# Performance work log

Hardware: AMD Instinct MI355X
Metric: run time of the kernel (lower is better)

The kernel has to match this reference:

```python
import jax, jax.numpy as jnp
import numpy as np

N_HEADS = 8

def setup_inputs() -> dict:
    key = jax.random.key(0)
    qkv = jax.random.normal(key, (4, 1536, 2048), dtype=jnp.float32)
    return {"qkv": qkv}

def reference(qkv):
    bs, width, length = qkv.shape
    ch = width // (3 * N_HEADS)
    q, k, v = jnp.split(qkv, 3, axis=1)  # each [bs, H*C, T]
    scale = 1.0 / np.sqrt(ch).astype(np.float32)
    q = (q * scale).reshape(bs * N_HEADS, ch, length)
    k = k.reshape(bs * N_HEADS, ch, length)
    v = v.reshape(bs * N_HEADS, ch, length)
    weight = jnp.einsum('bct,bcs->bts', q, k)  # [bs*H, T, T]
    weight = jax.nn.softmax(weight.astype(jnp.float32), axis=-1).astype(weight.dtype)
    a = jnp.einsum('bts,bcs->bct', weight, v)  # [bs*H, C, T]
    return a.reshape(bs, -1, length)
```

## Files before the change

kernel.cpp:

```cpp
#include <hip/hip_runtime.h>
#include <hip/hip_bf16.h>

typedef unsigned short u16;
typedef unsigned int uint;
typedef __bf16 bf16x8 __attribute__((ext_vector_type(8)));
typedef float f32x16 __attribute__((ext_vector_type(16)));

#define SEQ 2048
#define DH  64

__device__ __forceinline__ u16 f2bf(float x) {
  __bf16 h = (__bf16)x;
  return __builtin_bit_cast(u16, h);
}

__global__ __launch_bounds__(256) void transpose_qk(const float* __restrict__ qkv,
                                                    u16* __restrict__ qT,
                                                    u16* __restrict__ kT) {
  int idx = blockIdx.x;
  int which = idx >> 10;
  int bh = (idx >> 5) & 31;
  int t0 = (idx & 31) * 64;
  int b = bh >> 3, h = bh & 7;
  const float* src = qkv + ((size_t)(b*1536 + which*512 + h*64)) * SEQ;
  u16* dst = (which ? kT : qT) + (size_t)bh * SEQ * DH;
  float scale = which ? 1.0f : 0.1803368801111244f;

  __shared__ float tile[64][65];
  int tl = threadIdx.x & 63;
  int cw = threadIdx.x >> 6;
#pragma unroll
  for (int i = 0; i < 16; ++i) {
    int c = cw + 4*i;
    tile[c][tl] = src[(size_t)c*SEQ + t0 + tl] * scale;
  }
  __syncthreads();
  int cl2 = (threadIdx.x & 31) * 2;
  int tw  = threadIdx.x >> 5;
#pragma unroll
  for (int i = 0; i < 8; ++i) {
    int t = tw + 8*i;
    unsigned int lo = f2bf(tile[cl2][t]);
    unsigned int hi = f2bf(tile[cl2+1][t]);
    *(unsigned int*)(dst + (size_t)(t0 + t)*DH + cl2) = lo | (hi << 16);
  }
}

__global__ __launch_bounds__(256) void convert_v(const float* __restrict__ qkv,
                                                 u16* __restrict__ v) {
  int row = blockIdx.x;
  int bh = row >> 6, c = row & 63;
  int b = bh >> 3, h = bh & 7;
  const float4* src = (const float4*)(qkv + ((size_t)(b*1536 + 1024 + h*64 + c)) * SEQ);
  u16* dst = v + (size_t)row * SEQ;
  int tid = threadIdx.x;
  float4 a = src[tid*2];
  float4 bq = src[tid*2+1];
  union { u16 u[8]; int4 v4; } pk;
  pk.u[0]=f2bf(a.x); pk.u[1]=f2bf(a.y); pk.u[2]=f2bf(a.z); pk.u[3]=f2bf(a.w);
  pk.u[4]=f2bf(bq.x); pk.u[5]=f2bf(bq.y); pk.u[6]=f2bf(bq.z); pk.u[7]=f2bf(bq.w);
  *(int4*)(dst + tid*8) = pk.v4;
}

__global__ __launch_bounds__(256) void attn(const u16* __restrict__ qT,
                                            const u16* __restrict__ kT,
                                            const u16* __restrict__ vB,
                                            float* __restrict__ out) {
  const int lb = (blockIdx.x & 7) * 64 + (blockIdx.x >> 3);
  const int bh = lb >> 4;
  const int t0 = (lb & 15) * 128;
  const int tid  = threadIdx.x;
  const int wave = tid >> 6;
  const int lane = tid & 63;
  const int l31  = lane & 31;
  const int hi   = lane >> 5;

  __shared__ __align__(16) u16 kbuf[2][64*64];
  __shared__ __align__(16) u16 vbuf[2][64*64];

  const u16* qrow = qT + ((size_t)bh*SEQ + (t0 + wave*32 + l31)) * DH;
  bf16x8 bq[4];
#pragma unroll
  for (int kb = 0; kb < 4; ++kb) bq[kb] = *(const bf16x8*)(qrow + kb*16 + hi*8);

  const u16* ksrc0 = kT + (size_t)bh*SEQ*DH;
  const u16* vsrc0 = vB + (size_t)bh*DH*SEQ;
  const int ci0 = (wave*2+0)*64 + lane;
  const int ci1 = (wave*2+1)*64 + lane;
  const int kr0 = ci0 >> 3, kc0 = ci0 & 7;
  const int kr1 = ci1 >> 3, kc1 = ci1 & 7;
  const u16* kg0 = ksrc0 + (size_t)kr0*DH + ((kc0 ^ (kr0 & 7)) * 8);
  const u16* kg1 = ksrc0 + (size_t)kr1*DH + ((kc1 ^ (kr1 & 7)) * 8);
  const u16* vg0 = vsrc0 + (size_t)kr0*SEQ + ((kc0 ^ (kr0 & 7)) * 8);
  const u16* vg1 = vsrc0 + (size_t)kr1*SEQ + ((kc1 ^ (kr1 & 7)) * 8);

#define STAGE(b, s0) do {                                                         \
    __builtin_amdgcn_global_load_lds(                                             \
      (const __attribute__((address_space(1))) unsigned int*)(kg0 + (size_t)(s0)*DH), \
      (__attribute__((address_space(3))) unsigned int*)(&kbuf[b][(wave*2+0)*512]), 16, 0, 0); \
    __builtin_amdgcn_global_load_lds(                                             \
      (const __attribute__((address_space(1))) unsigned int*)(kg1 + (size_t)(s0)*DH), \
      (__attribute__((address_space(3))) unsigned int*)(&kbuf[b][(wave*2+1)*512]), 16, 0, 0); \
    __builtin_amdgcn_global_load_lds(                                             \
      (const __attribute__((address_space(1))) unsigned int*)(vg0 + (s0)),        \
      (__attribute__((address_space(3))) unsigned int*)(&vbuf[b][(wave*2+0)*512]), 16, 0, 0); \
    __builtin_amdgcn_global_load_lds(                                             \
      (const __attribute__((address_space(1))) unsigned int*)(vg1 + (s0)),        \
      (__attribute__((address_space(3))) unsigned int*)(&vbuf[b][(wave*2+1)*512]), 16, 0, 0); \
  } while (0)

  f32x16 acc0 = {}, acc1 = {};
  float m_run = -3.0e38f, l_run = 0.f;

  STAGE(0, 0);
  __syncthreads();

  int buf = 0;
  for (int s0 = 0; s0 < SEQ; s0 += 64) {
    if (s0 + 64 < SEQ) STAGE(buf ^ 1, s0 + 64);

    const u16* kb_ = kbuf[buf];
    f32x16 S0 = {}, S1 = {};
    __builtin_amdgcn_s_setprio(1);
#pragma unroll
    for (int kb = 0; kb < 4; ++kb) {
      bf16x8 a0 = *(const bf16x8*)(kb_ + l31*64      + (((2*kb+hi) ^ (l31 & 7)) * 8));
      bf16x8 a1 = *(const bf16x8*)(kb_ + (32+l31)*64 + (((2*kb+hi) ^ (l31 & 7)) * 8));
      S0 = __builtin_amdgcn_mfma_f32_32x32x16_bf16(a0, bq[kb], S0, 0, 0, 0);
      S1 = __builtin_amdgcn_mfma_f32_32x32x16_bf16(a1, bq[kb], S1, 0, 0, 0);
    }
    __builtin_amdgcn_s_setprio(0);

    float vmax = S0[0];
#pragma unroll
    for (int i = 1; i < 16; ++i) vmax = fmaxf(vmax, S0[i]);
#pragma unroll
    for (int i = 0; i < 16; ++i) vmax = fmaxf(vmax, S1[i]);
    vmax = fmaxf(vmax, __shfl_xor(vmax, 32));

    if (!__all(vmax - m_run <= 8.0f)) {
      float m_new = fmaxf(m_run, vmax);
      float alpha = __builtin_amdgcn_exp2f(m_run - m_new);
      l_run *= alpha;
#pragma unroll
      for (int i = 0; i < 16; ++i) { acc0[i] *= alpha; acc1[i] *= alpha; }
      m_run = m_new;
    }

    float p0[16], p1[16];
    float ls = 0.f;
#pragma unroll
    for (int i = 0; i < 16; ++i) { p0[i] = __builtin_amdgcn_exp2f(S0[i] - m_run); ls += p0[i]; }
#pragma unroll
    for (int i = 0; i < 16; ++i) { p1[i] = __builtin_amdgcn_exp2f(S1[i] - m_run); ls += p1[i]; }
    ls += __shfl_xor(ls, 32);
    l_run += ls;

    uint d0[8], d1[8];
#pragma unroll
    for (int q = 0; q < 4; ++q)
#pragma unroll
      for (int e = 0; e < 2; ++e) {
        asm("v_cvt_pk_bf16_f32 %0, %1, %2" : "=v"(d0[2*q+e]) : "v"(p0[4*q+2*e]), "v"(p0[4*q+2*e+1]));
        asm("v_cvt_pk_bf16_f32 %0, %1, %2" : "=v"(d1[2*q+e]) : "v"(p1[4*q+2*e]), "v"(p1[4*q+2*e+1]));
      }
    bf16x8 pf[4];
#pragma unroll
    for (int st2 = 0; st2 < 2; ++st2)
#pragma unroll
      for (int kb2 = 0; kb2 < 2; ++kb2) {
        uint X0 = (st2 ? d1 : d0)[4*kb2+0], X1 = (st2 ? d1 : d0)[4*kb2+1];
        uint Y0 = (st2 ? d1 : d0)[4*kb2+2], Y1 = (st2 ? d1 : d0)[4*kb2+3];
        asm("v_permlane32_swap_b32 %0, %1" : "+v"(X0), "+v"(Y0));
        asm("v_permlane32_swap_b32 %0, %1" : "+v"(X1), "+v"(Y1));
        uint4 u = {X0, X1, Y0, Y1};
        pf[st2*2+kb2] = __builtin_bit_cast(bf16x8, u);
      }

    const u16* vb_ = vbuf[buf];
    __builtin_amdgcn_s_setprio(1);
#pragma unroll
    for (int ks = 0; ks < 4; ++ks) {
      bf16x8 a0 = *(const bf16x8*)(vb_ + l31*64      + (((2*ks+hi) ^ (l31 & 7)) * 8));
      bf16x8 a1 = *(const bf16x8*)(vb_ + (32+l31)*64 + (((2*ks+hi) ^ (l31 & 7)) * 8));
      acc0 = __builtin_amdgcn_mfma_f32_32x32x16_bf16(a0, pf[ks], acc0, 0, 0, 0);
      acc1 = __builtin_amdgcn_mfma_f32_32x32x16_bf16(a1, pf[ks], acc1, 0, 0, 0);
    }
    __builtin_amdgcn_s_setprio(0);

    __syncthreads();
    buf ^= 1;
  }
#undef STAGE

  float linv = 1.0f / l_run;
  float* ob = out + (size_t)(bh*64) * SEQ + t0 + wave*32 + l31;
#pragma unroll
  for (int r = 0; r < 16; ++r) {
    int c0 = (r & 3) + 8*(r >> 2) + 4*hi;
    ob[(size_t)c0 * SEQ]        = acc0[r] * linv;
    ob[(size_t)(32 + c0) * SEQ] = acc1[r] * linv;
  }
}

extern "C" void kernel_launch(void* const* d_in, const int* in_sizes, int n_in,
                              void* d_out, int out_size, void* d_ws, size_t ws_size,
                              hipStream_t stream) {
  const float* qkv = (const float*)d_in[0];
  float* out = (float*)d_out;
  u16* qT = (u16*)d_ws;
  u16* kT = qT + (size_t)32*SEQ*DH;
  u16* vB = kT + (size_t)32*SEQ*DH;
  transpose_qk<<<2048, 256, 0, stream>>>(qkv, qT, kT);
  convert_v<<<2048, 256, 0, stream>>>(qkv, vB);
  attn<<<512, 256, 0, stream>>>(qT, kT, vB, out);
}
```

Measured before the change: 74.47 us.

## Halve attention block to two waves, double grid, change LDS swizzle, tree reductions

The attention kernel now runs 128-thread blocks covering 64 query rows each, with twice as many blocks. This is meant to spread work over more CUs and improve occupancy, at the cost of each block loading the K/V tiles for fewer queries and so doing more redundant global traffic. The K/V staging is rewritten so each wave issues four loads per tile, and the LDS XOR swizzle now uses a different function of the row index. The max and sum reductions become tree reductions to shorten their dependency chains.

```diff
diff --git a/kernel.cpp b/kernel.cpp
--- a/kernel.cpp
+++ b/kernel.cpp
@@ -13,6 +13,8 @@
   __bf16 h = (__bf16)x;
   return __builtin_bit_cast(u16, h);
 }
+
+#define FSW(r) ((((r) & 3) << 1) | (((r) >> 2) & 1))
 
 __global__ __launch_bounds__(256) void transpose_qk(const float* __restrict__ qkv,
                                                     u16* __restrict__ qT,
@@ -62,15 +64,15 @@
   *(int4*)(dst + tid*8) = pk.v4;
 }
 
-__global__ __launch_bounds__(256) void attn(const u16* __restrict__ qT,
+__global__ __launch_bounds__(128) void attn(const u16* __restrict__ qT,
                                             const u16* __restrict__ kT,
                                             const u16* __restrict__ vB,
                                             float* __restrict__ out) {
-  const int lb = (blockIdx.x & 7) * 64 + (blockIdx.x >> 3);
-  const int bh = lb >> 4;
-  const int t0 = (lb & 15) * 128;
+  const int lb = (blockIdx.x & 7) * 128 + (blockIdx.x >> 3);
+  const int bh = lb >> 5;
+  const int t0 = (lb & 31) * 64;
   const int tid  = threadIdx.x;
-  const int wave = tid >> 6;
+  const int wv   = tid >> 6;
   const int lane = tid & 63;
   const int l31  = lane & 31;
   const int hi   = lane >> 5;
@@ -78,39 +80,41 @@
   __shared__ __align__(16) u16 kbuf[2][64*64];
   __shared__ __align__(16) u16 vbuf[2][64*64];
 
-  const u16* qrow = qT + ((size_t)bh*SEQ + (t0 + wave*32 + l31)) * DH;
+  const u16* qrow = qT + ((size_t)bh*SEQ + (t0 + wv*32 + l31)) * DH;
   bf16x8 bq[4];
 #pragma unroll
   for (int kb = 0; kb < 4; ++kb) bq[kb] = *(const bf16x8*)(qrow + kb*16 + hi*8);
 
   const u16* ksrc0 = kT + (size_t)bh*SEQ*DH;
   const u16* vsrc0 = vB + (size_t)bh*DH*SEQ;
-  const int ci0 = (wave*2+0)*64 + lane;
-  const int ci1 = (wave*2+1)*64 + lane;
-  const int kr0 = ci0 >> 3, kc0 = ci0 & 7;
-  const int kr1 = ci1 >> 3, kc1 = ci1 & 7;
-  const u16* kg0 = ksrc0 + (size_t)kr0*DH + ((kc0 ^ (kr0 & 7)) * 8);
-  const u16* kg1 = ksrc0 + (size_t)kr1*DH + ((kc1 ^ (kr1 & 7)) * 8);
-  const u16* vg0 = vsrc0 + (size_t)kr0*SEQ + ((kc0 ^ (kr0 & 7)) * 8);
-  const u16* vg1 = vsrc0 + (size_t)kr1*SEQ + ((kc1 ^ (kr1 & 7)) * 8);
-
-#define STAGE(b, s0) do {                                                         \
-    __builtin_amdgcn_global_load_lds(                                             \
-      (const __attribute__((address_space(1))) unsigned int*)(kg0 + (size_t)(s0)*DH), \
-      (__attribute__((address_space(3))) unsigned int*)(&kbuf[b][(wave*2+0)*512]), 16, 0, 0); \
-    __builtin_amdgcn_global_load_lds(                                             \
-      (const __attribute__((address_space(1))) unsigned int*)(kg1 + (size_t)(s0)*DH), \
-      (__attribute__((address_space(3))) unsigned int*)(&kbuf[b][(wave*2+1)*512]), 16, 0, 0); \
-    __builtin_amdgcn_global_load_lds(                                             \
-      (const __attribute__((address_space(1))) unsigned int*)(vg0 + (s0)),        \
-      (__attribute__((address_space(3))) unsigned int*)(&vbuf[b][(wave*2+0)*512]), 16, 0, 0); \
-    __builtin_amdgcn_global_load_lds(                                             \
-      (const __attribute__((address_space(1))) unsigned int*)(vg1 + (s0)),        \
-      (__attribute__((address_space(3))) unsigned int*)(&vbuf[b][(wave*2+1)*512]), 16, 0, 0); \
+  const int r3  = lane >> 3;
+  const int kcc = lane & 7;
+  const int krb = wv*32 + r3;
+  const int fsw = FSW(r3);
+  const u16* kg  = ksrc0 + (size_t)krb*DH + ((kcc ^ fsw) * 8);
+  const u16* vg0 = vsrc0 + (size_t)(krb     )*SEQ + ((kcc ^ fsw) * 8);
+  const u16* vg1 = vsrc0 + (size_t)(krb +  8)*SEQ + ((kcc ^ fsw) * 8);
+  const u16* vg2 = vsrc0 + (size_t)(krb + 16)*SEQ + ((kcc ^ fsw) * 8);
+  const u16* vg3 = vsrc0 + (size_t)(krb + 24)*SEQ + ((kcc ^ fsw) * 8);
+
+#define GLDS(src, dst) __builtin_amdgcn_global_load_lds(                        \
+    (const __attribute__((address_space(1))) unsigned int*)(src),               \
+    (__attribute__((address_space(3))) unsigned int*)(dst), 16, 0, 0)
+#define STAGE(b, s0) do {                                                       \
+    GLDS(kg + (size_t)(s0)*DH,           &kbuf[b][(wv*4+0)*512]);               \
+    GLDS(kg + (size_t)(s0)*DH +  8*DH,   &kbuf[b][(wv*4+1)*512]);               \
+    GLDS(kg + (size_t)(s0)*DH + 16*DH,   &kbuf[b][(wv*4+2)*512]);               \
+    GLDS(kg + (size_t)(s0)*DH + 24*DH,   &kbuf[b][(wv*4+3)*512]);               \
+    GLDS(vg0 + (s0),                     &vbuf[b][(wv*4+0)*512]);               \
+    GLDS(vg1 + (s0),                     &vbuf[b][(wv*4+1)*512]);               \
+    GLDS(vg2 + (s0),                     &vbuf[b][(wv*4+2)*512]);               \
+    GLDS(vg3 + (s0),                     &vbuf[b][(wv*4+3)*512]);               \
   } while (0)
 
   f32x16 acc0 = {}, acc1 = {};
   float m_run = -3.0e38f, l_run = 0.f;
+
+  const int fl = FSW(l31);
 
   STAGE(0, 0);
   __syncthreads();
@@ -124,19 +128,22 @@
     __builtin_amdgcn_s_setprio(1);
 #pragma unroll
     for (int kb = 0; kb < 4; ++kb) {
-      bf16x8 a0 = *(const bf16x8*)(kb_ + l31*64      + (((2*kb+hi) ^ (l31 & 7)) * 8));
-      bf16x8 a1 = *(const bf16x8*)(kb_ + (32+l31)*64 + (((2*kb+hi) ^ (l31 & 7)) * 8));
+      bf16x8 a0 = *(const bf16x8*)(kb_ + l31*64      + (((2*kb+hi) ^ fl) * 8));
+      bf16x8 a1 = *(const bf16x8*)(kb_ + (32+l31)*64 + (((2*kb+hi) ^ fl) * 8));
       S0 = __builtin_amdgcn_mfma_f32_32x32x16_bf16(a0, bq[kb], S0, 0, 0, 0);
       S1 = __builtin_amdgcn_mfma_f32_32x32x16_bf16(a1, bq[kb], S1, 0, 0, 0);
     }
     __builtin_amdgcn_s_setprio(0);
 
-    float vmax = S0[0];
-#pragma unroll
-    for (int i = 1; i < 16; ++i) vmax = fmaxf(vmax, S0[i]);
-#pragma unroll
-    for (int i = 0; i < 16; ++i) vmax = fmaxf(vmax, S1[i]);
-    vmax = fmaxf(vmax, __shfl_xor(vmax, 32));
+    float mx[16];
+#pragma unroll
+    for (int i = 0; i < 16; ++i) mx[i] = fmaxf(S0[i], S1[i]);
+#pragma unroll
+    for (int i = 0; i < 8; ++i) mx[i] = fmaxf(mx[i], mx[i+8]);
+#pragma unroll
+    for (int i = 0; i < 4; ++i) mx[i] = fmaxf(mx[i], mx[i+4]);
+    mx[0] = fmaxf(fmaxf(mx[0], mx[1]), fmaxf(mx[2], mx[3]));
+    float vmax = fmaxf(mx[0], __shfl_xor(mx[0], 32));
 
     if (!__all(vmax - m_run <= 8.0f)) {
       float m_new = fmaxf(m_run, vmax);
@@ -148,11 +155,19 @@
     }
 
     float p0[16], p1[16];
-    float ls = 0.f;
-#pragma unroll
-    for (int i = 0; i < 16; ++i) { p0[i] = __builtin_amdgcn_exp2f(S0[i] - m_run); ls += p0[i]; }
-#pragma unroll
-    for (int i = 0; i < 16; ++i) { p1[i] = __builtin_amdgcn_exp2f(S1[i] - m_run); ls += p1[i]; }
+#pragma unroll
+    for (int i = 0; i < 16; ++i) p0[i] = __builtin_amdgcn_exp2f(S0[i] - m_run);
+#pragma unroll
+    for (int i = 0; i < 16; ++i) p1[i] = __builtin_amdgcn_exp2f(S1[i] - m_run);
+
+    float sm[16];
+#pragma unroll
+    for (int i = 0; i < 16; ++i) sm[i] = p0[i] + p1[i];
+#pragma unroll
+    for (int i = 0; i < 8; ++i) sm[i] += sm[i+8];
+#pragma unroll
+    for (int i = 0; i < 4; ++i) sm[i] += sm[i+4];
+    float ls = (sm[0] + sm[1]) + (sm[2] + sm[3]);
     ls += __shfl_xor(ls, 32);
     l_run += ls;
 
@@ -181,8 +196,8 @@
     __builtin_amdgcn_s_setprio(1);
 #pragma unroll
     for (int ks = 0; ks < 4; ++ks) {
-      bf16x8 a0 = *(const bf16x8*)(vb_ + l31*64      + (((2*ks+hi) ^ (l31 & 7)) * 8));
-      bf16x8 a1 = *(const bf16x8*)(vb_ + (32+l31)*64 + (((2*ks+hi) ^ (l31 & 7)) * 8));
+      bf16x8 a0 = *(const bf16x8*)(vb_ + l31*64      + (((2*ks+hi) ^ fl) * 8));
+      bf16x8 a1 = *(const bf16x8*)(vb_ + (32+l31)*64 + (((2*ks+hi) ^ fl) * 8));
       acc0 = __builtin_amdgcn_mfma_f32_32x32x16_bf16(a0, pf[ks], acc0, 0, 0, 0);
       acc1 = __builtin_amdgcn_mfma_f32_32x32x16_bf16(a1, pf[ks], acc1, 0, 0, 0);
     }
@@ -192,9 +207,10 @@
     buf ^= 1;
   }
 #undef STAGE
+#undef GLDS
 
   float linv = 1.0f / l_run;
-  float* ob = out + (size_t)(bh*64) * SEQ + t0 + wave*32 + l31;
+  float* ob = out + (size_t)(bh*64) * SEQ + t0 + wv*32 + l31;
 #pragma unroll
   for (int r = 0; r < 16; ++r) {
     int c0 = (r & 3) + 8*(r >> 2) + 4*hi;
@@ -213,5 +229,5 @@
   u16* vB = kT + (size_t)32*SEQ*DH;
   transpose_qk<<<2048, 256, 0, stream>>>(qkv, qT, kT);
   convert_v<<<2048, 256, 0, stream>>>(qkv, vB);
-  attn<<<512, 256, 0, stream>>>(qT, kT, vB, out);
-}
+  attn<<<1024, 128, 0, stream>>>(qT, kT, vB, out);
+}
```

New measurement: 79.77 us. 7.1% more time.
